# Kernel optimization log

Hardware: AMD Instinct MI355X
Metric: run time of the kernel (lower is better)

The kernel has to match this reference:

```python
import jax, jax.numpy as jnp
import numpy as np

HEADS = 8
DIM_HEAD = 64
DIM = 512
KERNEL = 33
SCALE = DIM_HEAD ** -0.5


def setup_inputs() -> dict:
    key = jax.random.key(0)
    k1, k2, k3, k4, k5, k6 = jax.random.split(key, 6)
    b, n = 2, 2048
    inner = HEADS * DIM_HEAD
    x = jax.random.normal(k1, (b, n, DIM), dtype=jnp.float32)
    mask = jax.random.uniform(k2, (b, n)) < 0.9
    W_qkv = jax.random.normal(k3, (DIM, inner * 3), dtype=jnp.float32) / np.sqrt(DIM)
    W_out = jax.random.normal(k4, (inner, DIM), dtype=jnp.float32) / np.sqrt(inner)
    b_out = jax.random.normal(k5, (DIM,), dtype=jnp.float32) * 0.01
    # depthwise Conv2d(heads, heads, (K,1), groups=heads) weight: (O=heads, I/groups=1, K, 1)
    conv_w = jax.random.normal(k6, (HEADS, 1, KERNEL, 1), dtype=jnp.float32) / np.sqrt(KERNEL)
    return {"x": x, "mask": mask, "W_qkv": W_qkv, "W_out": W_out,
            "b_out": b_out, "conv_w": conv_w}


def reference(x, mask, W_qkv, W_out, b_out, conv_w):
    b, n, _ = x.shape
    h, d = HEADS, DIM_HEAD
    qkv = (x @ W_qkv).reshape(b, n, 3, h, d)          # chunk(3) then (h d) split
    q = qkv[:, :, 0].transpose(0, 2, 1, 3)            # b h n d
    k = qkv[:, :, 1].transpose(0, 2, 1, 3)
    v = qkv[:, :, 2].transpose(0, 2, 1, 3)
    dots = jnp.einsum('bhid,bhjd->bhij', q, k) * SCALE
    mask_value = -jnp.finfo(dots.dtype).max
    dots = jnp.where(mask[:, None, None, :], dots, mask_value)
    attn = jax.nn.softmax(dots, axis=-1)
    out = jnp.einsum('bhij,bhjd->bhid', attn, v)      # b h n d
    # depthwise residual conv over sequence axis (height), per head
    pad = KERNEL // 2
    res = jax.lax.conv_general_dilated(
        v, conv_w, window_strides=(1, 1), padding=((pad, pad), (0, 0)),
        dimension_numbers=('NCHW', 'OIHW', 'NCHW'), feature_group_count=h)
    out = out + res
    out = out.transpose(0, 2, 1, 3).reshape(b, n, h * d)  # b n (h d)
    out = out @ W_out + b_out
    out = jnp.where(mask[:, :, None], out, 0.0)
    return out
```

## Files before the change

kernel.cpp:

```cpp
#include <hip/hip_runtime.h>
#include <float.h>

#define BATCH 2
#define SEQ   2048
#define HEADS 8
#define DHEAD 64
#define DIMM  512
#define NQKV  1536
#define QK_SCALE 0.125f
#define QSCALE_L2 (0.125f * 1.44269504f)

#define QKV_ELEMS ((size_t)BATCH * HEADS * SEQ * DHEAD)

typedef __bf16 bf16x8 __attribute__((ext_vector_type(8)));
typedef short  s16x4  __attribute__((ext_vector_type(4)));
typedef float  f32x4  __attribute__((ext_vector_type(4)));

#if __has_builtin(__builtin_amdgcn_exp2f)
#define EXP2F __builtin_amdgcn_exp2f
#else
#define EXP2F exp2f
#endif

__device__ __forceinline__ unsigned short bfbits(float f) {
  __bf16 h = (__bf16)f;
  return *(unsigned short*)&h;
}
__device__ __forceinline__ float bf2f(unsigned short u) {
  return __uint_as_float((unsigned)u << 16);
}
__device__ __forceinline__ unsigned cvtpk(float a, float b) {
  unsigned r;
  asm("v_cvt_pk_bf16_f32 %0, %1, %2" : "=v"(r) : "v"(a), "v"(b));
  return r;
}
__device__ __forceinline__ f32x4 mfma16(s16x4 a, s16x4 b, f32x4 c) {
#if __has_builtin(__builtin_amdgcn_mfma_f32_16x16x16bf16_1k)
  return __builtin_amdgcn_mfma_f32_16x16x16bf16_1k(a, b, c, 0, 0, 0);
#else
  f32x4 d;
  asm("v_mfma_f32_16x16x16_bf16 %0, %1, %2, %3" : "=v"(d) : "v"(a), "v"(b), "v"(c));
  return d;
#endif
}

__global__ __launch_bounds__(1024) void prep_mask(const void* __restrict__ mraw,
                                                  float* __restrict__ maskf,
                                                  unsigned* __restrict__ kmaxn) {
  __shared__ int f_bf16, f_f32, f_gt1, f_oddnz;
  const int t = threadIdx.x;
  if (t < 16) kmaxn[t] = 0u;
  if (t == 0) { f_bf16 = 0; f_f32 = 0; f_gt1 = 0; f_oddnz = 0; }
  __syncthreads();
  const unsigned int* w = (const unsigned int*)mraw;
  unsigned int v = w[t];
  if (v == 0x3f803f80u) f_bf16 = 1;
  if (v == 0x3f800000u) f_f32 = 1;
  if (v > 1u)           f_gt1 = 1;
  if ((t & 1) && v != 0u) f_oddnz = 1;
  __syncthreads();
  int mode;
  if (f_bf16)       mode = 4;
  else if (f_f32)   mode = 3;
  else if (f_gt1)   mode = 1;
  else if (!f_oddnz) mode = 2;
  else              mode = 0;
  for (int i = t; i < BATCH * SEQ; i += 1024) {
    bool keep;
    if (mode == 4)      keep = ((const unsigned short*)mraw)[i] != 0;
    else if (mode == 3) keep = ((const float*)mraw)[i] != 0.f;
    else if (mode == 1) keep = ((const unsigned char*)mraw)[i] != 0;
    else if (mode == 2) keep = w[2 * i] != 0u;
    else                keep = w[i] != 0u;
    maskf[i] = keep ? 1.f : 0.f;
  }
}

__global__ __launch_bounds__(256) void x_to_bf16(const float* __restrict__ X,
                                                 unsigned short* __restrict__ Xbf) {
  size_t i = ((size_t)blockIdx.x * 256 + threadIdx.x) * 8;
  float4 a0 = *(const float4*)(X + i);
  float4 a1 = *(const float4*)(X + i + 4);
  union { unsigned short u[8]; int4 v; } pk;
  pk.u[0] = bfbits(a0.x); pk.u[1] = bfbits(a0.y);
  pk.u[2] = bfbits(a0.z); pk.u[3] = bfbits(a0.w);
  pk.u[4] = bfbits(a1.x); pk.u[5] = bfbits(a1.y);
  pk.u[6] = bfbits(a1.z); pk.u[7] = bfbits(a1.w);
  *(int4*)(Xbf + i) = pk.v;
}

__global__ __launch_bounds__(256) void transpose_w(const float* __restrict__ W,
                                                   unsigned short* __restrict__ Wt,
                                                   int K, int N) {
  __shared__ float T[64][65];
  const int t = threadIdx.x;
  const int n0 = blockIdx.x * 64, k0 = blockIdx.y * 64;
  {
    int r0 = t >> 4, c4 = t & 15;
#pragma unroll
    for (int rr = 0; rr < 4; ++rr) {
      int r = r0 + rr * 16;
      float4 v = *(const float4*)(W + (size_t)(k0 + r) * N + n0 + c4 * 4);
      T[r][c4 * 4 + 0] = v.x; T[r][c4 * 4 + 1] = v.y;
      T[r][c4 * 4 + 2] = v.z; T[r][c4 * 4 + 3] = v.w;
    }
  }
  __syncthreads();
  {
    int n = t >> 2, kc = t & 3;
    union { unsigned short u[16]; int4 v[2]; } p;
#pragma unroll
    for (int i = 0; i < 16; ++i) p.u[i] = bfbits(T[kc * 16 + i][n]);
    int4* dst = (int4*)(Wt + (size_t)(n0 + n) * K + k0 + kc * 16);
    dst[0] = p.v[0]; dst[1] = p.v[1];
  }
}

__global__ __launch_bounds__(256) void gemm_qkv_mfma(
    const unsigned short* __restrict__ Xbf, const unsigned short* __restrict__ Wt,
    unsigned short* __restrict__ Qbf, unsigned short* __restrict__ Kbf,
    unsigned short* __restrict__ Vt) {
  __shared__ __align__(16) unsigned char Al[128 * 128];
  __shared__ __align__(16) unsigned char Bl[64 * 128];
  const int tid = threadIdx.x;
  const int lane = tid & 63;
  const int w = tid >> 6;
  const int l15 = lane & 15, g = lane >> 4;
  const int wr = w >> 1, wc = w & 1;
  int bid = blockIdx.x;
  int lid = (bid & 7) * 96 + (bid >> 3);
  int by = lid / 24, bx = lid - by * 24;
  const int m0 = by * 128;

  f32x4 acc[4][2] = {};
  const int srow = tid >> 3, scg = tid & 7;
  const int rsw = (l15 & 7) << 4;

  for (int k0 = 0; k0 < DIMM; k0 += 64) {
    __syncthreads();
#pragma unroll
    for (int it = 0; it < 4; ++it) {
      int row = srow + it * 32;
      int sw = (row & 7) << 4;
      *(int4*)(Al + row * 128 + ((scg * 16) ^ sw)) =
          *(const int4*)(Xbf + (size_t)(m0 + row) * DIMM + k0 + scg * 8);
      if (it < 2) {
        *(int4*)(Bl + row * 128 + ((scg * 16) ^ sw)) =
            *(const int4*)(Wt + (size_t)(bx * 64 + row) * DIMM + k0 + scg * 8);
      }
    }
    __syncthreads();
#pragma unroll
    for (int ks = 0; ks < 2; ++ks) {
      bf16x8 af[4], bfr[2];
#pragma unroll
      for (int mi = 0; mi < 4; ++mi)
        af[mi] = *(const bf16x8*)(Al + (wr * 64 + mi * 16 + l15) * 128 +
                                  ((ks * 64 + g * 16) ^ rsw));
#pragma unroll
      for (int nj = 0; nj < 2; ++nj)
        bfr[nj] = *(const bf16x8*)(Bl + (wc * 32 + nj * 16 + l15) * 128 +
                                   ((ks * 64 + g * 16) ^ rsw));
#pragma unroll
      for (int mi = 0; mi < 4; ++mi)
#pragma unroll
        for (int nj = 0; nj < 2; ++nj)
          acc[mi][nj] = __builtin_amdgcn_mfma_f32_16x16x32_bf16(
              af[mi], bfr[nj], acc[mi][nj], 0, 0, 0);
    }
  }
  const int chunk = bx >> 3;
  const int bb = m0 >> 11;
#pragma unroll
  for (int nj = 0; nj < 2; ++nj) {
    int col = (bx & 7) * 64 + wc * 32 + nj * 16 + l15;
    int hh = col >> 6, dd = col & 63;
#pragma unroll
    for (int mi = 0; mi < 4; ++mi) {
      int ii0 = (m0 & (SEQ - 1)) + wr * 64 + mi * 16 + g * 4;
      if (chunk == 2) {
        union { unsigned short u[4]; ushort4 v; } pk;
#pragma unroll
        for (int r = 0; r < 4; ++r) pk.u[r] = bfbits(acc[mi][nj][r]);
        *(ushort4*)(Vt + ((size_t)(bb * HEADS + hh) * DHEAD + dd) * SEQ + ii0) = pk.v;
      } else {
        unsigned short* dst = (chunk == 0) ? Qbf : Kbf;
        float sc = (chunk == 0) ? QSCALE_L2 : 1.f;
#pragma unroll
        for (int r = 0; r < 4; ++r)
          dst[((size_t)(bb * HEADS + hh) * SEQ + ii0 + r) * DHEAD + dd] =
              bfbits(acc[mi][nj][r] * sc);
      }
    }
  }
}

__global__ __launch_bounds__(256) void knorm(const unsigned short* __restrict__ Kbf,
                                             unsigned* __restrict__ kmaxn) {
  int row = blockIdx.x * 256 + threadIdx.x;
  const bf16x8* kr = (const bf16x8*)(Kbf + (size_t)row * DHEAD);
  float n2 = 0.f;
#pragma unroll
  for (int c = 0; c < 8; ++c) {
    bf16x8 v = kr[c];
#pragma unroll
    for (int i = 0; i < 8; ++i) { float f = (float)v[i]; n2 += f * f; }
  }
#pragma unroll
  for (int d = 1; d < 64; d <<= 1) n2 = fmaxf(n2, __shfl_xor(n2, d));
  if ((threadIdx.x & 63) == 0)
    atomicMax(kmaxn + (row >> 11), __float_as_uint(n2));
}

__global__ __launch_bounds__(256) void attn_split(const unsigned short* __restrict__ Qbf,
                                                  const unsigned short* __restrict__ Kbf,
                                                  const unsigned short* __restrict__ Vt,
                                                  const float* __restrict__ maskf,
                                                  const unsigned* __restrict__ kmaxn,
                                                  unsigned short* __restrict__ Po,
                                                  float* __restrict__ LSE) {
  __shared__ __align__(16) unsigned char Ks[8192];
  __shared__ __align__(16) unsigned char Vs[8192];
  __shared__ __align__(16) float skm[64];

  const int tid = threadIdx.x;
  const int lane = tid & 63;
  const int w = tid >> 6;
  const int l15 = lane & 15, g = lane >> 4;

  int fid = blockIdx.x;
  int lid = (fid & 7) * 128 + (fid >> 3);
  const int bh = lid >> 6;
  const int rem = lid & 63;
  const int qb = rem >> 1;
  const int half = rem & 1;
  const int bb = bh >> 3;

  const unsigned short* Qg = Qbf + ((size_t)bh * SEQ + qb * 64) * DHEAD;
  const unsigned short* Kg = Kbf + (size_t)bh * SEQ * DHEAD;
  const unsigned short* Vg = Vt  + (size_t)bh * DHEAD * SEQ;

  bf16x8 qf0, qf1;
  {
    const unsigned char* qrow = (const unsigned char*)(Qg + (size_t)(w * 16 + l15) * DHEAD);
    qf0 = *(const bf16x8*)(qrow + g * 16);
    qf1 = *(const bf16x8*)(qrow + 64 + g * 16);
  }
  float Bx, Bnat;
  {
    float qn2 = 0.f;
#pragma unroll
    for (int i = 0; i < 8; ++i) {
      float a = (float)qf0[i]; qn2 += a * a;
      float b = (float)qf1[i]; qn2 += b * b;
    }
    qn2 += __shfl_xor(qn2, 16);
    qn2 += __shfl_xor(qn2, 32);
    const float kmax2 = __uint_as_float(kmaxn[bh]);
    Bx = sqrtf(qn2 * kmax2);
    Bnat = Bx * 0.69314718f;
  }

  f32x4 o[4] = {};
  float lsum = 0.f;

  const int sm = tid >> 2;
  const int sc = (tid & 3) * 32;
  const int ssw = (sm & 7) << 4;
  const int rsw = (l15 & 7) << 4;

  const int kt0 = half * 16;
  int4 rk0, rk1, rv0, rv1;
  float rmv = 0.f;
  {
    const unsigned char* ksrc =
        (const unsigned char*)(Kg + (size_t)kt0 * 64 * DHEAD) + sm * 128 + sc;
    const unsigned char* vsrc =
        (const unsigned char*)(Vg + (size_t)sm * SEQ + kt0 * 64) + sc;
    rk0 = *(const int4*)(ksrc); rk1 = *(const int4*)(ksrc + 16);
    rv0 = *(const int4*)(vsrc); rv1 = *(const int4*)(vsrc + 16);
    if (tid < 64) rmv = maskf[bb * SEQ + kt0 * 64 + tid];
  }

  for (int kt = kt0; kt < kt0 + 16; ++kt) {
    __syncthreads();
    *(int4*)(Ks + sm * 128 + ((sc)      ^ ssw)) = rk0;
    *(int4*)(Ks + sm * 128 + ((sc + 16) ^ ssw)) = rk1;
    *(int4*)(Vs + sm * 128 + ((sc)      ^ ssw)) = rv0;
    *(int4*)(Vs + sm * 128 + ((sc + 16) ^ ssw)) = rv1;
    if (tid < 64) skm[tid] = rmv;
    if (kt + 1 < kt0 + 16) {
      const unsigned char* ksrc =
          (const unsigned char*)(Kg + (size_t)(kt + 1) * 64 * DHEAD) + sm * 128 + sc;
      const unsigned char* vsrc =
          (const unsigned char*)(Vg + (size_t)sm * SEQ + (kt + 1) * 64) + sc;
      rk0 = *(const int4*)(ksrc); rk1 = *(const int4*)(ksrc + 16);
      rv0 = *(const int4*)(vsrc); rv1 = *(const int4*)(vsrc + 16);
      if (tid < 64) rmv = maskf[bb * SEQ + (kt + 1) * 64 + tid];
    }
    __syncthreads();

    f32x4 s[4];
#pragma unroll
    for (int j = 0; j < 4; ++j) {
      const unsigned char* krow = Ks + (16 * j + l15) * 128;
      bf16x8 kf0 = *(const bf16x8*)(krow + ((g * 16)      ^ rsw));
      bf16x8 kf1 = *(const bf16x8*)(krow + ((64 + g * 16) ^ rsw));
      f32x4 z = (f32x4){0.f, 0.f, 0.f, 0.f};
      z = __builtin_amdgcn_mfma_f32_16x16x32_bf16(kf0, qf0, z, 0, 0, 0);
      z = __builtin_amdgcn_mfma_f32_16x16x32_bf16(kf1, qf1, z, 0, 0, 0);
      s[j] = z;
    }

    s16x4 pa[4];
#pragma unroll
    for (int j = 0; j < 4; ++j) {
      float4 km4 = *(const float4*)&skm[16 * j + 4 * g];
      float p0 = EXP2F(s[j][0] - Bx) * km4.x;
      float p1 = EXP2F(s[j][1] - Bx) * km4.y;
      float p2 = EXP2F(s[j][2] - Bx) * km4.z;
      float p3 = EXP2F(s[j][3] - Bx) * km4.w;
      lsum += (p0 + p1) + (p2 + p3);
      union { uint2 u; s16x4 v; } pk;
      pk.u.x = cvtpk(p0, p1);
      pk.u.y = cvtpk(p2, p3);
      pa[j] = pk.v;
    }

#pragma unroll
    for (int dj = 0; dj < 4; ++dj) {
      const unsigned char* vrow = Vs + (16 * dj + l15) * 128;
#pragma unroll
      for (int j = 0; j < 4; ++j) {
        s16x4 vb = *(const s16x4*)(vrow + ((32 * j + 8 * g) ^ rsw));
        o[dj] = mfma16(pa[j], vb, o[dj]);
      }
    }
  }

  lsum += __shfl_xor(lsum, 16);
  lsum += __shfl_xor(lsum, 32);
#pragma unroll
  for (int r = 0; r < 4; ++r) {
    float lr = __shfl(lsum, 4 * g + r);
    float inv = (lr > 0.f) ? 1.f / lr : 0.f;
    int row = qb * 64 + w * 16 + 4 * g + r;
    size_t base = half * QKV_ELEMS + ((size_t)bh * SEQ + row) * DHEAD + l15;
    Po[base]      = bfbits(o[0][r] * inv);
    Po[base + 16] = bfbits(o[1][r] * inv);
    Po[base + 32] = bfbits(o[2][r] * inv);
    Po[base + 48] = bfbits(o[3][r] * inv);
  }
  if (g == 0) {
    int row = qb * 64 + w * 16 + l15;
    LSE[half * (BATCH * HEADS * SEQ) + bh * SEQ + row] =
        (lsum > 0.f) ? Bnat + __logf(lsum) : -3.0e38f;
  }
}

__global__ __launch_bounds__(256) void combine_conv(
    const unsigned short* __restrict__ Po, const float* __restrict__ LSE,
    const unsigned short* __restrict__ Vt, const float* __restrict__ cw,
    unsigned short* __restrict__ Obf) {
  __shared__ float T[96][68];
  __shared__ float cwl[33];
  const int tid = threadIdx.x;
  const int bid = blockIdx.x;
  const int bh = bid >> 5;
  const int n0 = (bid & 31) * 64;
  const int hh = bh & 7;
  if (tid < 33) cwl[tid] = cw[hh * 33 + tid];
  for (int idx = tid; idx < 64 * 24; idx += 256) {
    int d = idx / 24, c4 = idx - (idx / 24) * 24;
    int nbase = n0 - 16 + c4 * 4;
    const unsigned short* src = Vt + ((size_t)bh * DHEAD + d) * SEQ;
#pragma unroll
    for (int q = 0; q < 4; ++q) {
      int n = nbase + q;
      T[c4 * 4 + q][d] = (n >= 0 && n < SEQ) ? bf2f(src[n]) : 0.f;
    }
  }
  __syncthreads();
#pragma unroll
  for (int p = 0; p < 4; ++p) {
    int n = (tid >> 4) + p * 16;
    int d4 = tid & 15;
    int row = bh * SEQ + n0 + n;
    float ls0 = LSE[row], ls1 = LSE[BATCH * HEADS * SEQ + row];
    float m = fmaxf(ls0, ls1);
    float w0 = __expf(ls0 - m), w1 = __expf(ls1 - m);
    float inv = 1.f / (w0 + w1);
    w0 *= inv; w1 *= inv;
    const unsigned short* p0 = Po + (size_t)row * DHEAD + d4 * 4;
    const unsigned short* p1 = p0 + QKV_ELEMS;
    ushort4 a = *(const ushort4*)p0, b = *(const ushort4*)p1;
    float o0 = w0 * bf2f(a.x) + w1 * bf2f(b.x);
    float o1 = w0 * bf2f(a.y) + w1 * bf2f(b.y);
    float o2 = w0 * bf2f(a.z) + w1 * bf2f(b.z);
    float o3 = w0 * bf2f(a.w) + w1 * bf2f(b.w);
#pragma unroll
    for (int t = 0; t < 33; ++t) {
      float wv = cwl[t];
      float4 tv = *(const float4*)&T[n + t][d4 * 4];
      o0 += wv * tv.x; o1 += wv * tv.y; o2 += wv * tv.z; o3 += wv * tv.w;
    }
    union { unsigned short u[4]; ushort4 v; } pk;
    pk.u[0] = bfbits(o0); pk.u[1] = bfbits(o1);
    pk.u[2] = bfbits(o2); pk.u[3] = bfbits(o3);
    *(ushort4*)(Obf + (size_t)row * DHEAD + d4 * 4) = pk.v;
  }
}

__global__ __launch_bounds__(256) void gemm_out_mfma(
    const unsigned short* __restrict__ Obf, const unsigned short* __restrict__ Wt,
    const float* __restrict__ bias, const float* __restrict__ maskf,
    float* __restrict__ out) {
  __shared__ __align__(16) unsigned char Al[64 * 128];
  __shared__ __align__(16) unsigned char Bl[64 * 128];
  const int tid = threadIdx.x;
  const int lane = tid & 63;
  const int w = tid >> 6;
  const int l15 = lane & 15, g = lane >> 4;
  const int wr = w >> 1, wc = w & 1;
  int bid = blockIdx.x;
  int lid = (bid & 7) * 64 + (bid >> 3);
  int by = lid >> 3, bx = lid & 7;
  const int m0 = by * 64, n0 = bx * 64;
  const int bb = m0 >> 11;
  const int ii0 = m0 & (SEQ - 1);

  f32x4 acc[2][2] = {};
  const int srow = tid >> 3, scg = tid & 7;
  const int rsw = (l15 & 7) << 4;

  for (int k0 = 0; k0 < DIMM; k0 += 64) {
    const int hh = k0 >> 6;
    __syncthreads();
#pragma unroll
    for (int it = 0; it < 2; ++it) {
      int row = srow + it * 32;
      int sw = (row & 7) << 4;
      *(int4*)(Al + row * 128 + ((scg * 16) ^ sw)) =
          *(const int4*)(Obf + ((size_t)(bb * HEADS + hh) * SEQ + ii0 + row) * DHEAD + scg * 8);
      *(int4*)(Bl + row * 128 + ((scg * 16) ^ sw)) =
          *(const int4*)(Wt + (size_t)(n0 + row) * DIMM + k0 + scg * 8);
    }
    __syncthreads();
#pragma unroll
    for (int ks = 0; ks < 2; ++ks) {
      bf16x8 af[2], bfr[2];
#pragma unroll
      for (int mi = 0; mi < 2; ++mi)
        af[mi] = *(const bf16x8*)(Al + (wr * 32 + mi * 16 + l15) * 128 +
                                  ((ks * 64 + g * 16) ^ rsw));
#pragma unroll
      for (int nj = 0; nj < 2; ++nj)
        bfr[nj] = *(const bf16x8*)(Bl + (wc * 32 + nj * 16 + l15) * 128 +
                                   ((ks * 64 + g * 16) ^ rsw));
#pragma unroll
      for (int mi = 0; mi < 2; ++mi)
#pragma unroll
        for (int nj = 0; nj < 2; ++nj)
          acc[mi][nj] = __builtin_amdgcn_mfma_f32_16x16x32_bf16(
              af[mi], bfr[nj], acc[mi][nj], 0, 0, 0);
    }
  }
#pragma unroll
  for (int nj = 0; nj < 2; ++nj) {
    int col = n0 + wc * 32 + nj * 16 + l15;
    float bcol = bias[col];
#pragma unroll
    for (int mi = 0; mi < 2; ++mi) {
#pragma unroll
      for (int r = 0; r < 4; ++r) {
        int m = m0 + wr * 32 + mi * 16 + g * 4 + r;
        out[(size_t)m * DIMM + col] = (acc[mi][nj][r] + bcol) * maskf[m];
      }
    }
  }
}

extern "C" void kernel_launch(void* const* d_in, const int* in_sizes, int n_in,
                              void* d_out, int out_size, void* d_ws, size_t ws_size,
                              hipStream_t stream) {
  const float* x     = (const float*)d_in[0];
  const void*  mask  = d_in[1];
  const float* Wqkv  = (const float*)d_in[2];
  const float* Wout  = (const float*)d_in[3];
  const float* bout  = (const float*)d_in[4];
  const float* convw = (const float*)d_in[5];
  float* out = (float*)d_out;

  float* maskf = (float*)d_ws;
  unsigned* kmaxn = (unsigned*)(maskf + 4096);
  unsigned short* Qbf = (unsigned short*)(kmaxn + 64);
  unsigned short* Kbf = Qbf + QKV_ELEMS;
  unsigned short* Vt  = Kbf + QKV_ELEMS;
  unsigned short* Po  = Vt + QKV_ELEMS;
  float* LSE          = (float*)(Po + 2 * QKV_ELEMS);
  unsigned short* Obf = (unsigned short*)(LSE + 2 * BATCH * HEADS * SEQ);
  unsigned short* Wtq = Obf + QKV_ELEMS;
  unsigned short* Wto = Wtq + (size_t)NQKV * DIMM;
  unsigned short* Xbf = Wto + (size_t)DIMM * DIMM;

  prep_mask<<<1, 1024, 0, stream>>>(mask, maskf, kmaxn);
  x_to_bf16<<<1024, 256, 0, stream>>>(x, Xbf);
  transpose_w<<<dim3(NQKV / 64, DIMM / 64), 256, 0, stream>>>(Wqkv, Wtq, DIMM, NQKV);
  transpose_w<<<dim3(DIMM / 64, DIMM / 64), 256, 0, stream>>>(Wout, Wto, DIMM, DIMM);
  gemm_qkv_mfma<<<768, 256, 0, stream>>>(Xbf, Wtq, Qbf, Kbf, Vt);
  knorm<<<(BATCH * HEADS * SEQ) / 256, 256, 0, stream>>>(Kbf, kmaxn);
  attn_split<<<1024, 256, 0, stream>>>(Qbf, Kbf, Vt, maskf, kmaxn, Po, LSE);
  combine_conv<<<512, 256, 0, stream>>>(Po, LSE, Vt, convw, Obf);
  gemm_out_mfma<<<512, 256, 0, stream>>>(Obf, Wto, bout, maskf, out);
}
```

Measured before the change: 102.0 us.

## Merge prep kernels, fold K bound into QKV GEMM, double-buffer attention LDS

Merges the mask, x-conversion and both weight-transpose kernels into one launch. The knorm kernel is dropped; the QKV GEMM epilogue now records a per-head max |K| via atomicMax, and attention derives its softmax bound as sqrt(qn2)*8*max|K|, which is looser than before. The attention inner loop gains double-buffered K/V tiles in shared memory with one barrier per tile, and reads mask values straight from global memory. These changes cut launch overhead, remove a separate pass over K and halve barriers, at the cost of more LDS per block and a looser bound that may underflow exp2 for some rows.

Result: no change. 100.4 us (-1.5%).

```diff
diff --git a/kernel.cpp b/kernel.cpp
--- a/kernel.cpp
+++ b/kernel.cpp
@@ -7,7 +7,6 @@
 #define DHEAD 64
 #define DIMM  512
 #define NQKV  1536
-#define QK_SCALE 0.125f
 #define QSCALE_L2 (0.125f * 1.44269504f)
 
 #define QKV_ELEMS ((size_t)BATCH * HEADS * SEQ * DHEAD)
@@ -44,57 +43,9 @@
 #endif
 }
 
-__global__ __launch_bounds__(1024) void prep_mask(const void* __restrict__ mraw,
-                                                  float* __restrict__ maskf,
-                                                  unsigned* __restrict__ kmaxn) {
-  __shared__ int f_bf16, f_f32, f_gt1, f_oddnz;
-  const int t = threadIdx.x;
-  if (t < 16) kmaxn[t] = 0u;
-  if (t == 0) { f_bf16 = 0; f_f32 = 0; f_gt1 = 0; f_oddnz = 0; }
-  __syncthreads();
-  const unsigned int* w = (const unsigned int*)mraw;
-  unsigned int v = w[t];
-  if (v == 0x3f803f80u) f_bf16 = 1;
-  if (v == 0x3f800000u) f_f32 = 1;
-  if (v > 1u)           f_gt1 = 1;
-  if ((t & 1) && v != 0u) f_oddnz = 1;
-  __syncthreads();
-  int mode;
-  if (f_bf16)       mode = 4;
-  else if (f_f32)   mode = 3;
-  else if (f_gt1)   mode = 1;
-  else if (!f_oddnz) mode = 2;
-  else              mode = 0;
-  for (int i = t; i < BATCH * SEQ; i += 1024) {
-    bool keep;
-    if (mode == 4)      keep = ((const unsigned short*)mraw)[i] != 0;
-    else if (mode == 3) keep = ((const float*)mraw)[i] != 0.f;
-    else if (mode == 1) keep = ((const unsigned char*)mraw)[i] != 0;
-    else if (mode == 2) keep = w[2 * i] != 0u;
-    else                keep = w[i] != 0u;
-    maskf[i] = keep ? 1.f : 0.f;
-  }
-}
-
-__global__ __launch_bounds__(256) void x_to_bf16(const float* __restrict__ X,
-                                                 unsigned short* __restrict__ Xbf) {
-  size_t i = ((size_t)blockIdx.x * 256 + threadIdx.x) * 8;
-  float4 a0 = *(const float4*)(X + i);
-  float4 a1 = *(const float4*)(X + i + 4);
-  union { unsigned short u[8]; int4 v; } pk;
-  pk.u[0] = bfbits(a0.x); pk.u[1] = bfbits(a0.y);
-  pk.u[2] = bfbits(a0.z); pk.u[3] = bfbits(a0.w);
-  pk.u[4] = bfbits(a1.x); pk.u[5] = bfbits(a1.y);
-  pk.u[6] = bfbits(a1.z); pk.u[7] = bfbits(a1.w);
-  *(int4*)(Xbf + i) = pk.v;
-}
-
-__global__ __launch_bounds__(256) void transpose_w(const float* __restrict__ W,
-                                                   unsigned short* __restrict__ Wt,
-                                                   int K, int N) {
-  __shared__ float T[64][65];
-  const int t = threadIdx.x;
-  const int n0 = blockIdx.x * 64, k0 = blockIdx.y * 64;
+__device__ __forceinline__ void transpose_tile_dev(
+    const float* __restrict__ W, unsigned short* __restrict__ Wt,
+    int K, int N, int n0, int k0, int t, float T[64][65]) {
   {
     int r0 = t >> 4, c4 = t & 15;
 #pragma unroll
@@ -116,10 +67,65 @@
   }
 }
 
+__global__ __launch_bounds__(256) void prep_all(
+    const float* __restrict__ X, const void* __restrict__ mraw,
+    const float* __restrict__ Wqkv, const float* __restrict__ Wout,
+    unsigned short* __restrict__ Xbf, float* __restrict__ maskf,
+    unsigned short* __restrict__ Wtq, unsigned short* __restrict__ Wto,
+    unsigned* __restrict__ kmaxn) {
+  __shared__ float T[64][65];
+  __shared__ int f_bf16, f_f32, f_gt1, f_oddnz;
+  const int b = blockIdx.x;
+  const int t = threadIdx.x;
+  if (b < 1024) {
+    size_t i = ((size_t)b * 256 + t) * 8;
+    float4 a0 = *(const float4*)(X + i);
+    float4 a1 = *(const float4*)(X + i + 4);
+    union { unsigned short u[8]; int4 v; } pk;
+    pk.u[0] = bfbits(a0.x); pk.u[1] = bfbits(a0.y);
+    pk.u[2] = bfbits(a0.z); pk.u[3] = bfbits(a0.w);
+    pk.u[4] = bfbits(a1.x); pk.u[5] = bfbits(a1.y);
+    pk.u[6] = bfbits(a1.z); pk.u[7] = bfbits(a1.w);
+    *(int4*)(Xbf + i) = pk.v;
+  } else if (b < 1216) {
+    int bb2 = b - 1024;
+    transpose_tile_dev(Wqkv, Wtq, DIMM, NQKV, (bb2 % 24) * 64, (bb2 / 24) * 64, t, T);
+  } else if (b < 1280) {
+    int bb2 = b - 1216;
+    transpose_tile_dev(Wout, Wto, DIMM, DIMM, (bb2 & 7) * 64, (bb2 >> 3) * 64, t, T);
+  } else {
+    if (t < 16) kmaxn[t] = 0u;
+    if (t == 0) { f_bf16 = 0; f_f32 = 0; f_gt1 = 0; f_oddnz = 0; }
+    __syncthreads();
+    const unsigned int* w = (const unsigned int*)mraw;
+    unsigned int v = w[t];
+    if (v == 0x3f803f80u) f_bf16 = 1;
+    if (v == 0x3f800000u) f_f32 = 1;
+    if (v > 1u)           f_gt1 = 1;
+    if ((t & 1) && v != 0u) f_oddnz = 1;
+    __syncthreads();
+    int mode;
+    if (f_bf16)       mode = 4;
+    else if (f_f32)   mode = 3;
+    else if (f_gt1)   mode = 1;
+    else if (!f_oddnz) mode = 2;
+    else              mode = 0;
+    for (int i = t; i < BATCH * SEQ; i += 256) {
+      bool keep;
+      if (mode == 4)      keep = ((const unsigned short*)mraw)[i] != 0;
+      else if (mode == 3) keep = ((const float*)mraw)[i] != 0.f;
+      else if (mode == 1) keep = ((const unsigned char*)mraw)[i] != 0;
+      else if (mode == 2) keep = w[2 * i] != 0u;
+      else                keep = w[i] != 0u;
+      maskf[i] = keep ? 1.f : 0.f;
+    }
+  }
+}
+
 __global__ __launch_bounds__(256) void gemm_qkv_mfma(
     const unsigned short* __restrict__ Xbf, const unsigned short* __restrict__ Wt,
     unsigned short* __restrict__ Qbf, unsigned short* __restrict__ Kbf,
-    unsigned short* __restrict__ Vt) {
+    unsigned short* __restrict__ Vt, unsigned* __restrict__ kmaxn) {
   __shared__ __align__(16) unsigned char Al[128 * 128];
   __shared__ __align__(16) unsigned char Bl[64 * 128];
   const int tid = threadIdx.x;
@@ -193,23 +199,19 @@
       }
     }
   }
-}
-
-__global__ __launch_bounds__(256) void knorm(const unsigned short* __restrict__ Kbf,
-                                             unsigned* __restrict__ kmaxn) {
-  int row = blockIdx.x * 256 + threadIdx.x;
-  const bf16x8* kr = (const bf16x8*)(Kbf + (size_t)row * DHEAD);
-  float n2 = 0.f;
-#pragma unroll
-  for (int c = 0; c < 8; ++c) {
-    bf16x8 v = kr[c];
-#pragma unroll
-    for (int i = 0; i < 8; ++i) { float f = (float)v[i]; n2 += f * f; }
-  }
-#pragma unroll
-  for (int d = 1; d < 64; d <<= 1) n2 = fmaxf(n2, __shfl_xor(n2, d));
-  if ((threadIdx.x & 63) == 0)
-    atomicMax(kmaxn + (row >> 11), __float_as_uint(n2));
+  if (chunk == 1) {
+    float kab = 0.f;
+#pragma unroll
+    for (int nj = 0; nj < 2; ++nj)
+#pragma unroll
+      for (int mi = 0; mi < 4; ++mi)
+#pragma unroll
+        for (int r = 0; r < 4; ++r) kab = fmaxf(kab, fabsf(acc[mi][nj][r]));
+#pragma unroll
+    for (int d = 1; d < 64; d <<= 1) kab = fmaxf(kab, __shfl_xor(kab, d));
+    if (lane == 0)
+      atomicMax(kmaxn + (bb * HEADS + (bx & 7)), __float_as_uint(kab * 1.005f));
+  }
 }
 
 __global__ __launch_bounds__(256) void attn_split(const unsigned short* __restrict__ Qbf,
@@ -219,9 +221,8 @@
                                                   const unsigned* __restrict__ kmaxn,
                                                   unsigned short* __restrict__ Po,
                                                   float* __restrict__ LSE) {
-  __shared__ __align__(16) unsigned char Ks[8192];
-  __shared__ __align__(16) unsigned char Vs[8192];
-  __shared__ __align__(16) float skm[64];
+  __shared__ __align__(16) unsigned char Ks[16384];
+  __shared__ __align__(16) unsigned char Vs[16384];
 
   const int tid = threadIdx.x;
   const int lane = tid & 63;
@@ -239,6 +240,7 @@
   const unsigned short* Qg = Qbf + ((size_t)bh * SEQ + qb * 64) * DHEAD;
   const unsigned short* Kg = Kbf + (size_t)bh * SEQ * DHEAD;
   const unsigned short* Vg = Vt  + (size_t)bh * DHEAD * SEQ;
+  const float* mrow = maskf + bb * SEQ;
 
   bf16x8 qf0, qf1;
   {
@@ -256,8 +258,8 @@
     }
     qn2 += __shfl_xor(qn2, 16);
     qn2 += __shfl_xor(qn2, 32);
-    const float kmax2 = __uint_as_float(kmaxn[bh]);
-    Bx = sqrtf(qn2 * kmax2);
+    const float kabs = __uint_as_float(kmaxn[bh]);
+    Bx = sqrtf(qn2) * 8.f * kabs;
     Bnat = Bx * 0.69314718f;
   }
 
@@ -268,10 +270,9 @@
   const int sc = (tid & 3) * 32;
   const int ssw = (sm & 7) << 4;
   const int rsw = (l15 & 7) << 4;
-
   const int kt0 = half * 16;
+
   int4 rk0, rk1, rv0, rv1;
-  float rmv = 0.f;
   {
     const unsigned char* ksrc =
         (const unsigned char*)(Kg + (size_t)kt0 * 64 * DHEAD) + sm * 128 + sc;
@@ -279,31 +280,33 @@
         (const unsigned char*)(Vg + (size_t)sm * SEQ + kt0 * 64) + sc;
     rk0 = *(const int4*)(ksrc); rk1 = *(const int4*)(ksrc + 16);
     rv0 = *(const int4*)(vsrc); rv1 = *(const int4*)(vsrc + 16);
-    if (tid < 64) rmv = maskf[bb * SEQ + kt0 * 64 + tid];
-  }
-
-  for (int kt = kt0; kt < kt0 + 16; ++kt) {
-    __syncthreads();
-    *(int4*)(Ks + sm * 128 + ((sc)      ^ ssw)) = rk0;
-    *(int4*)(Ks + sm * 128 + ((sc + 16) ^ ssw)) = rk1;
-    *(int4*)(Vs + sm * 128 + ((sc)      ^ ssw)) = rv0;
-    *(int4*)(Vs + sm * 128 + ((sc + 16) ^ ssw)) = rv1;
-    if (tid < 64) skm[tid] = rmv;
-    if (kt + 1 < kt0 + 16) {
+  }
+  *(int4*)(Ks + sm * 128 + ((sc)      ^ ssw)) = rk0;
+  *(int4*)(Ks + sm * 128 + ((sc + 16) ^ ssw)) = rk1;
+  *(int4*)(Vs + sm * 128 + ((sc)      ^ ssw)) = rv0;
+  *(int4*)(Vs + sm * 128 + ((sc + 16) ^ ssw)) = rv1;
+  __syncthreads();
+
+  for (int t = 0; t < 16; ++t) {
+    const int kt = kt0 + t;
+    const int co = (t & 1) << 13;
+    const int no = co ^ 8192;
+    float4 km[4];
+#pragma unroll
+    for (int j = 0; j < 4; ++j) km[j] = *(const float4*)(mrow + kt * 64 + 16 * j + 4 * g);
+    if (t < 15) {
       const unsigned char* ksrc =
           (const unsigned char*)(Kg + (size_t)(kt + 1) * 64 * DHEAD) + sm * 128 + sc;
       const unsigned char* vsrc =
           (const unsigned char*)(Vg + (size_t)sm * SEQ + (kt + 1) * 64) + sc;
       rk0 = *(const int4*)(ksrc); rk1 = *(const int4*)(ksrc + 16);
       rv0 = *(const int4*)(vsrc); rv1 = *(const int4*)(vsrc + 16);
-      if (tid < 64) rmv = maskf[bb * SEQ + (kt + 1) * 64 + tid];
-    }
-    __syncthreads();
+    }
 
     f32x4 s[4];
 #pragma unroll
     for (int j = 0; j < 4; ++j) {
-      const unsigned char* krow = Ks + (16 * j + l15) * 128;
+      const unsigned char* krow = Ks + co + (16 * j + l15) * 128;
       bf16x8 kf0 = *(const bf16x8*)(krow + ((g * 16)      ^ rsw));
       bf16x8 kf1 = *(const bf16x8*)(krow + ((64 + g * 16) ^ rsw));
       f32x4 z = (f32x4){0.f, 0.f, 0.f, 0.f};
@@ -315,11 +318,10 @@
     s16x4 pa[4];
 #pragma unroll
     for (int j = 0; j < 4; ++j) {
-      float4 km4 = *(const float4*)&skm[16 * j + 4 * g];
-      float p0 = EXP2F(s[j][0] - Bx) * km4.x;
-      float p1 = EXP2F(s[j][1] - Bx) * km4.y;
-      float p2 = EXP2F(s[j][2] - Bx) * km4.z;
-      float p3 = EXP2F(s[j][3] - Bx) * km4.w;
+      float p0 = EXP2F(s[j][0] - Bx) * km[j].x;
+      float p1 = EXP2F(s[j][1] - Bx) * km[j].y;
+      float p2 = EXP2F(s[j][2] - Bx) * km[j].z;
+      float p3 = EXP2F(s[j][3] - Bx) * km[j].w;
       lsum += (p0 + p1) + (p2 + p3);
       union { uint2 u; s16x4 v; } pk;
       pk.u.x = cvtpk(p0, p1);
@@ -329,12 +331,20 @@
 
 #pragma unroll
     for (int dj = 0; dj < 4; ++dj) {
-      const unsigned char* vrow = Vs + (16 * dj + l15) * 128;
+      const unsigned char* vrow = Vs + co + (16 * dj + l15) * 128;
 #pragma unroll
       for (int j = 0; j < 4; ++j) {
         s16x4 vb = *(const s16x4*)(vrow + ((32 * j + 8 * g) ^ rsw));
         o[dj] = mfma16(pa[j], vb, o[dj]);
       }
+    }
+
+    if (t < 15) {
+      *(int4*)(Ks + no + sm * 128 + ((sc)      ^ ssw)) = rk0;
+      *(int4*)(Ks + no + sm * 128 + ((sc + 16) ^ ssw)) = rk1;
+      *(int4*)(Vs + no + sm * 128 + ((sc)      ^ ssw)) = rv0;
+      *(int4*)(Vs + no + sm * 128 + ((sc + 16) ^ ssw)) = rv1;
+      __syncthreads();
     }
   }
 
@@ -503,12 +513,8 @@
   unsigned short* Wto = Wtq + (size_t)NQKV * DIMM;
   unsigned short* Xbf = Wto + (size_t)DIMM * DIMM;
 
-  prep_mask<<<1, 1024, 0, stream>>>(mask, maskf, kmaxn);
-  x_to_bf16<<<1024, 256, 0, stream>>>(x, Xbf);
-  transpose_w<<<dim3(NQKV / 64, DIMM / 64), 256, 0, stream>>>(Wqkv, Wtq, DIMM, NQKV);
-  transpose_w<<<dim3(DIMM / 64, DIMM / 64), 256, 0, stream>>>(Wout, Wto, DIMM, DIMM);
-  gemm_qkv_mfma<<<768, 256, 0, stream>>>(Xbf, Wtq, Qbf, Kbf, Vt);
-  knorm<<<(BATCH * HEADS * SEQ) / 256, 256, 0, stream>>>(Kbf, kmaxn);
+  prep_all<<<1281, 256, 0, stream>>>(x, mask, Wqkv, Wout, Xbf, maskf, Wtq, Wto, kmaxn);
+  gemm_qkv_mfma<<<768, 256, 0, stream>>>(Xbf, Wtq, Qbf, Kbf, Vt, kmaxn);
   attn_split<<<1024, 256, 0, stream>>>(Qbf, Kbf, Vt, maskf, kmaxn, Po, LSE);
   combine_conv<<<512, 256, 0, stream>>>(Po, LSE, Vt, convw, Obf);
   gemm_out_mfma<<<512, 256, 0, stream>>>(Obf, Wto, bout, maskf, out);
```
